# Optimization experiments

Hardware: AMD Instinct MI355X
Metric: run time of the kernel (lower is better)

## Reference

```python
import jax, jax.numpy as jnp
import numpy as np

H = 16  # num_heads


def setup_inputs() -> dict:
    key = jax.random.key(0)
    ks = jax.random.split(key, 8)
    B, S, d, L = 1, 2048, 1024, 8
    hd = d // H
    s = 0.02
    return {
        "x": jax.random.normal(ks[0], (B, S, d), jnp.float32),
        "past_values": jax.random.normal(ks[1], (L, B, H, S, hd), jnp.float32),
        "Wqkv": jax.random.normal(ks[2], (3 * d, d), jnp.float32) * s,
        "bqkv": jax.random.normal(ks[3], (3 * d,), jnp.float32) * s,
        "Wcol": jax.random.normal(ks[4], (d, d), jnp.float32) * s,
        "bcol": jax.random.normal(ks[5], (d,), jnp.float32) * s,
        "Wout": jax.random.normal(ks[6], (d, d), jnp.float32) * s,
        "bout": jax.random.normal(ks[7], (d,), jnp.float32) * s,
    }


def reference(x, past_values, Wqkv, bqkv, Wcol, bcol, Wout, bout):
    B, S, d = x.shape
    L = past_values.shape[0]
    hd = d // H
    scale = 1.0 / np.sqrt(hd).astype(np.float32)

    qkv = x @ Wqkv.T + bqkv                       # [B,S,3d]
    q, k, v = jnp.split(qkv, 3, axis=-1)

    def heads(t):                                  # [B,S,d] -> [B,H,S,hd]
        return t.reshape(B, S, H, hd).transpose(0, 2, 1, 3)

    q_row, k, v = heads(q), heads(k), heads(v)
    q_col = heads(x @ Wcol.T + bcol)

    # causal token scores [B,H,S,S]
    token_scores = jnp.einsum('bhqd,bhkd->bhqk', q_row, k) * scale
    causal = jnp.triu(jnp.ones((S, S), bool), 1)
    token_scores = jnp.where(causal, -jnp.inf, token_scores)

    # stack past values: torch stack(dim=3) -> [B,H,S,L,hd]; permute -> [B,S,L,H*hd]
    pv = past_values.transpose(1, 3, 0, 2, 4).reshape(B, S, L, d)
    ri = pv.reshape(B, S * L, d)
    mu = ri.mean(-1, keepdims=True)
    var = ri.var(-1, keepdims=True)
    ri = (ri - mu) / jnp.sqrt(var + 1e-5)          # F.layer_norm, no affine

    Wk, bk = Wqkv[d:2 * d], bqkv[d:2 * d]
    Wv, bv = Wqkv[2 * d:], bqkv[2 * d:]
    rk = (ri @ Wk.T + bk).reshape(B, S * L, H, hd).transpose(0, 2, 1, 3).reshape(B, H, S, L, hd)
    rv = (ri @ Wv.T + bv).reshape(B, S * L, H, hd).transpose(0, 2, 1, 3).reshape(B, H, S, L, hd)

    mem_scores = jnp.einsum('bhsd,bhsld->bhsl', q_col, rk) * scale  # [B,H,S,L]

    scores = jnp.concatenate([token_scores, mem_scores], axis=-1)   # [B,H,S,S+L]
    w = jax.nn.softmax(scores, axis=-1)
    tw, mw = w[..., :S], w[..., S:]

    ctx = jnp.einsum('bhqk,bhkd->bhqd', tw, v) + jnp.einsum('bhsl,bhsld->bhsd', mw, rv)
    out = ctx.transpose(0, 2, 1, 3).reshape(B, S, d)
    return out @ Wout.T + bout
```

## Files before the change

kernel.cpp:

```cpp
#include <hip/hip_runtime.h>
#include <math.h>

#define D   1024
#define H   16
#define HD  64
#define SEQ 2048
#define LL  8
#define SCALE 0.125f
#define TZS 1048

typedef __attribute__((ext_vector_type(8))) __bf16 bf16x8;
typedef __attribute__((ext_vector_type(4))) float floatx4;
typedef __attribute__((ext_vector_type(8))) unsigned short ushort8;

__device__ inline unsigned short f32_to_bf16(float f) {
    unsigned int u = __builtin_bit_cast(unsigned int, f);
    u += 0x7FFF + ((u >> 16) & 1);
    return (unsigned short)(u >> 16);
}
__device__ inline float bf2f(unsigned short u) {
    unsigned int x = (unsigned int)u << 16;
    return __builtin_bit_cast(float, x);
}
__device__ inline void load_lds16(const void* g, void* l) {
    __builtin_amdgcn_global_load_lds(
        (__attribute__((address_space(1))) void*)g,
        (__attribute__((address_space(3))) void*)l, 16, 0, 0);
}
__device__ inline void xcd_swizzle(int& bx, int& by) {
    const int gx   = gridDim.x;
    const int lin  = blockIdx.y * gx + blockIdx.x;
    const int nblk = gx * gridDim.y;
    const int virt = (lin & 7) * (nblk >> 3) + (lin >> 3);
    bx = virt % gx;
    by = virt / gx;
}

#define NQ_X    524288
#define NQ_WQKV 786432
#define NQ_WC   262144
#define LN_BLK  16384
#define CVT_BLK 7168
#define TR_BLK  256
#define PREP_GRID (LN_BLK + CVT_BLK + 4 + TR_BLK)

__global__ __launch_bounds__(256) void prep_kernel(
    const float* __restrict__ pv, const float* __restrict__ x,
    const float* __restrict__ Wqkv, const float* __restrict__ Wcol,
    const float* __restrict__ Wout, const float* __restrict__ bqkv,
    const float* __restrict__ bcol,
    unsigned short* __restrict__ ri, unsigned short* __restrict__ xb,
    unsigned short* __restrict__ W4b, unsigned short* __restrict__ Woutb,
    float* __restrict__ b4, unsigned short* __restrict__ WkT)
{
    __shared__ float ft[64][65];
    const int b = blockIdx.x;
    const int t = threadIdx.x;
    if (b < LN_BLK) {
        const int r = b;
        const int s = r >> 3, l = r & 7;
        const int h = t >> 4, e = (t & 15) * 4;
        const size_t src = (size_t)l * (H * SEQ * HD) + (size_t)h * (SEQ * HD)
                         + (size_t)s * HD + e;
        float4 v = *(const float4*)(pv + src);
        float sum = v.x + v.y + v.z + v.w;
        float sq  = v.x * v.x + v.y * v.y + v.z * v.z + v.w * v.w;
#pragma unroll
        for (int off = 32; off; off >>= 1) {
            sum += __shfl_xor(sum, off);
            sq  += __shfl_xor(sq, off);
        }
        __shared__ float red[8];
        if ((t & 63) == 0) { red[(t >> 6) * 2] = sum; red[(t >> 6) * 2 + 1] = sq; }
        __syncthreads();
        sum = red[0] + red[2] + red[4] + red[6];
        sq  = red[1] + red[3] + red[5] + red[7];
        const float mean = sum * (1.f / 1024.f);
        const float var  = sq * (1.f / 1024.f) - mean * mean;
        const float rstd = rsqrtf(var + 1e-5f);
        ushort4 o;
        o.x = f32_to_bf16((v.x - mean) * rstd);
        o.y = f32_to_bf16((v.y - mean) * rstd);
        o.z = f32_to_bf16((v.z - mean) * rstd);
        o.w = f32_to_bf16((v.w - mean) * rstd);
        *(ushort4*)(ri + (size_t)r * D + t * 4) = o;
    } else if (b < LN_BLK + CVT_BLK) {
        const int i = (b - LN_BLK) * 256 + t;
        const float* src; unsigned short* dst; int off;
        if (i < NQ_X) {
            src = x; dst = xb; off = i;
        } else if (i < NQ_X + NQ_WQKV) {
            src = Wqkv; dst = W4b; off = i - NQ_X;
        } else if (i < NQ_X + NQ_WQKV + NQ_WC) {
            src = Wcol; dst = W4b + (size_t)NQ_WQKV * 4; off = i - NQ_X - NQ_WQKV;
        } else {
            src = Wout; dst = Woutb; off = i - NQ_X - NQ_WQKV - NQ_WC;
        }
        float4 v = ((const float4*)src)[off];
        ushort4 o;
        o.x = f32_to_bf16(v.x); o.y = f32_to_bf16(v.y);
        o.z = f32_to_bf16(v.z); o.w = f32_to_bf16(v.w);
        ((ushort4*)dst)[off] = o;
    } else if (b < LN_BLK + CVT_BLK + 4) {
        const int q = (b - LN_BLK - CVT_BLK) * 256 + t;
        float4 v = (q < 768) ? ((const float4*)bqkv)[q] : ((const float4*)bcol)[q - 768];
        ((float4*)b4)[q] = v;
    } else {
        const int tt = b - LN_BLK - CVT_BLK - 4;
        const int kt = tt >> 4, et = tt & 15;
        const int r = t >> 2, c16 = (t & 3) * 16;
        const float* srow = Wqkv + (size_t)(1024 + et * 64 + r) * 1024 + kt * 64 + c16;
#pragma unroll
        for (int j = 0; j < 4; j++) {
            float4 v = *(const float4*)(srow + j * 4);
            ft[r][c16 + j * 4 + 0] = v.x; ft[r][c16 + j * 4 + 1] = v.y;
            ft[r][c16 + j * 4 + 2] = v.z; ft[r][c16 + j * 4 + 3] = v.w;
        }
        __syncthreads();
        const int rk = t >> 2, ec = (t & 3) * 16;
        unsigned short* orow = WkT + (size_t)(kt * 64 + rk) * 1024 + et * 64 + ec;
#pragma unroll
        for (int half = 0; half < 2; half++) {
            ushort8 o;
#pragma unroll
            for (int j = 0; j < 8; j++)
                o[j] = f32_to_bf16(ft[ec + half * 8 + j][rk]);
            *(ushort8*)(orow + half * 8) = o;
        }
    }
}

template <typename CT>
__global__ __launch_bounds__(256) void gemm_bf16_kernel(
    const unsigned short* __restrict__ A, const unsigned short* __restrict__ W,
    const float* __restrict__ bias, CT* __restrict__ C, int K, int N)
{
    __shared__ unsigned short As[128 * 32];
    __shared__ unsigned short Ws[128 * 32];
    const int t    = threadIdx.x;
    const int wave = t >> 6, lane = t & 63;
    const int wm   = wave >> 1, wn = wave & 1;
    int bx, by;
    xcd_swizzle(bx, by);
    const int m0 = by * 128, n0 = bx * 128;

    floatx4 acc[4][4];
#pragma unroll
    for (int i = 0; i < 4; i++)
#pragma unroll
        for (int j = 0; j < 4; j++) acc[i][j] = (floatx4)0.f;

    const int lrow = lane >> 2;
    const int lcol = (lane & 3) * 8;
    const unsigned short* Ag = A + (size_t)(m0 + wave * 32 + lrow) * K + lcol;
    const unsigned short* Wg = W + (size_t)(n0 + wave * 32 + lrow) * K + lcol;
    unsigned short* Asw = &As[wave * 32 * 32];
    unsigned short* Wsw = &Ws[wave * 32 * 32];
    const size_t rowskip = (size_t)16 * K;

    const int arow  = lane & 15;
    const int aquad = (lane >> 4) * 8;

    for (int k0 = 0; k0 < K; k0 += 32) {
        load_lds16(Ag + k0,           Asw);
        load_lds16(Ag + k0 + rowskip, Asw + 16 * 32);
        load_lds16(Wg + k0,           Wsw);
        load_lds16(Wg + k0 + rowskip, Wsw + 16 * 32);
        __syncthreads();

        bf16x8 af[4], wf[4];
#pragma unroll
        for (int mi = 0; mi < 4; mi++)
            af[mi] = *(const bf16x8*)&As[(wm * 64 + mi * 16 + arow) * 32 + aquad];
#pragma unroll
        for (int ni = 0; ni < 4; ni++)
            wf[ni] = *(const bf16x8*)&Ws[(wn * 64 + ni * 16 + arow) * 32 + aquad];
#pragma unroll
        for (int mi = 0; mi < 4; mi++)
#pragma unroll
            for (int ni = 0; ni < 4; ni++)
                acc[mi][ni] = __builtin_amdgcn_mfma_f32_16x16x32_bf16(
                    af[mi], wf[ni], acc[mi][ni], 0, 0, 0);
        __syncthreads();
    }

    const int crow = (lane >> 4) * 4, ccol = lane & 15;
#pragma unroll
    for (int mi = 0; mi < 4; mi++) {
#pragma unroll
        for (int ni = 0; ni < 4; ni++) {
            const int gm = m0 + wm * 64 + mi * 16 + crow;
            const int gn = n0 + wn * 64 + ni * 16 + ccol;
            const float bb = bias[gn];
#pragma unroll
            for (int r = 0; r < 4; r++) {
                float v = acc[mi][ni][r] + bb;
                if constexpr (sizeof(CT) == 2)
                    C[(size_t)(gm + r) * N + gn] = (CT)f32_to_bf16(v);
                else
                    C[(size_t)(gm + r) * N + gn] = v;
            }
        }
    }
}

__global__ __launch_bounds__(256, 2) void mem_attn_kernel(
    const unsigned short* __restrict__ qkv4, const unsigned short* __restrict__ ri,
    const unsigned short* __restrict__ WkT, const unsigned short* __restrict__ Wv,
    const float* __restrict__ bk, const float* __restrict__ bv,
    float* __restrict__ Omem, float2* __restrict__ mlmem)
{
    const int t = threadIdx.x;
    const int w = t >> 6, lane = t & 63;
    const int lrow = lane & 15, quad = lane >> 4, lk = quad * 8;
    const int b  = blockIdx.x;
    const int sg = (b & 7) + 8 * ((b >> 3) & 15);
    const int hg = b >> 7;
    const int s0 = sg * 16;
    const int r0 = s0 * 8;

    __shared__ unsigned short tz[2][16][TZS];
    __shared__ float s_sc[2][16][8];
    __shared__ float s_c[2][16];
    __shared__ float s_p[2][16][8];
    __shared__ float s_l2[2][16];

    {
        const int hh = t >> 7, s = (t >> 3) & 15, g = t & 7;
        const int h = hg * 2 + hh;
        const unsigned short* qc = qkv4 + (size_t)(s0 + s) * 4096 + 3072 + h * 64 + g * 8;
        ushort8 qv = *(const ushort8*)qc;
        float acc = 0.f;
#pragma unroll
        for (int j = 0; j < 8; j++)
            acc += bf2f(qv[j]) * bk[h * 64 + g * 8 + j];
        acc += __shfl_xor(acc, 1);
        acc += __shfl_xor(acc, 2);
        acc += __shfl_xor(acc, 4);
        if (g == 0) s_c[hh][s] = acc;
    }

    bf16x8 aq[2][2];
#pragma unroll
    for (int hh = 0; hh < 2; hh++)
#pragma unroll
        for (int kst = 0; kst < 2; kst++)
            aq[hh][kst] = *(const bf16x8*)(qkv4 + (size_t)(s0 + lrow) * 4096 + 3072
                                           + (hg * 2 + hh) * 64 + kst * 32 + lk);
#pragma unroll
    for (int hh = 0; hh < 2; hh++) {
        const int h = hg * 2 + hh;
#pragma unroll
        for (int nt = 0; nt < 16; nt++) {
            const int n = w * 256 + nt * 16;
            floatx4 acc = (floatx4)0.f;
#pragma unroll
            for (int kst = 0; kst < 2; kst++) {
                bf16x8 bw = *(const bf16x8*)(WkT + (size_t)(n + lrow) * 1024
                                             + h * 64 + kst * 32 + lk);
                acc = __builtin_amdgcn_mfma_f32_16x16x32_bf16(aq[hh][kst], bw, acc, 0, 0, 0);
            }
#pragma unroll
            for (int r = 0; r < 4; r++)
                tz[hh][quad * 4 + r][n + lrow] = f32_to_bf16(acc[r]);
        }
    }
    __syncthreads();

    {
        floatx4 sacc[2][2];
#pragma unroll
        for (int ntl = 0; ntl < 2; ntl++)
#pragma unroll
            for (int hh = 0; hh < 2; hh++) sacc[ntl][hh] = (floatx4)0.f;
        for (int kst = 0; kst < 32; kst++) {
            bf16x8 at0 = *(const bf16x8*)&tz[0][lrow][kst * 32 + lk];
            bf16x8 at1 = *(const bf16x8*)&tz[1][lrow][kst * 32 + lk];
#pragma unroll
            for (int ntl = 0; ntl < 2; ntl++) {
                bf16x8 br = *(const bf16x8*)(ri + (size_t)(r0 + w * 32 + ntl * 16 + lrow) * 1024
                                             + kst * 32 + lk);
                sacc[ntl][0] = __builtin_amdgcn_mfma_f32_16x16x32_bf16(at0, br, sacc[ntl][0], 0, 0, 0);
                sacc[ntl][1] = __builtin_amdgcn_mfma_f32_16x16x32_bf16(at1, br, sacc[ntl][1], 0, 0, 0);
            }
        }
        if (quad == w) {
            const int l = lrow & 7, hi = (lrow >> 3) & 1;
#pragma unroll
            for (int ntl = 0; ntl < 2; ntl++) {
                const int s = 4 * w + 2 * ntl + hi;
#pragma unroll
                for (int hh = 0; hh < 2; hh++) {
                    float val = hi ? sacc[ntl][hh][2 * ntl + 1] : sacc[ntl][hh][2 * ntl];
                    s_sc[hh][s][l] = val;
                }
            }
        }
    }
    __syncthreads();

    if (t < 32) {
        const int hh = t >> 4, s = t & 15;
        const int h = hg * 2 + hh;
        const float c = s_c[hh][s];
        float sc[8], m2 = -1e30f;
#pragma unroll
        for (int l = 0; l < 8; l++) {
            sc[l] = (s_sc[hh][s][l] + c) * SCALE;
            m2 = fmaxf(m2, sc[l]);
        }
        float l2 = 0.f;
#pragma unroll
        for (int l = 0; l < 8; l++) {
            float p = __expf(sc[l] - m2);
            s_p[hh][s][l] = p;
            l2 += p;
        }
        s_l2[hh][s] = l2;
        mlmem[(size_t)h * 2048 + s0 + s] = make_float2(m2, l2);
    }
    __syncthreads();

    {
        const int s = t & 15, kc = (t >> 4) * 64;
        float z0[64], z1[64];
#pragma unroll
        for (int j = 0; j < 64; j++) { z0[j] = 0.f; z1[j] = 0.f; }
        for (int l = 0; l < 8; l++) {
            const float p0 = s_p[0][s][l], p1 = s_p[1][s][l];
            const unsigned short* base = ri + (size_t)(r0 + s * 8 + l) * 1024 + kc;
#pragma unroll
            for (int c8 = 0; c8 < 8; c8++) {
                ushort8 v = *(const ushort8*)(base + c8 * 8);
#pragma unroll
                for (int j = 0; j < 8; j++) {
                    float f = bf2f(v[j]);
                    z0[c8 * 8 + j] = fmaf(p0, f, z0[c8 * 8 + j]);
                    z1[c8 * 8 + j] = fmaf(p1, f, z1[c8 * 8 + j]);
                }
            }
        }
        __syncthreads();
#pragma unroll
        for (int c8 = 0; c8 < 8; c8++) {
            ushort8 o0, o1;
#pragma unroll
            for (int j = 0; j < 8; j++) {
                o0[j] = f32_to_bf16(z0[c8 * 8 + j]);
                o1[j] = f32_to_bf16(z1[c8 * 8 + j]);
            }
            *(ushort8*)&tz[0][s][kc + c8 * 8] = o0;
            *(ushort8*)&tz[1][s][kc + c8 * 8] = o1;
        }
    }
    __syncthreads();

    {
        floatx4 oacc[2] = {(floatx4)0.f, (floatx4)0.f};
        for (int kst = 0; kst < 32; kst++) {
            bf16x8 az0 = *(const bf16x8*)&tz[0][lrow][kst * 32 + lk];
            bf16x8 az1 = *(const bf16x8*)&tz[1][lrow][kst * 32 + lk];
            bf16x8 bw0 = *(const bf16x8*)(Wv + (size_t)((hg * 2 + 0) * 64 + w * 16 + lrow) * 1024
                                          + kst * 32 + lk);
            bf16x8 bw1 = *(const bf16x8*)(Wv + (size_t)((hg * 2 + 1) * 64 + w * 16 + lrow) * 1024
                                          + kst * 32 + lk);
            oacc[0] = __builtin_amdgcn_mfma_f32_16x16x32_bf16(az0, bw0, oacc[0], 0, 0, 0);
            oacc[1] = __builtin_amdgcn_mfma_f32_16x16x32_bf16(az1, bw1, oacc[1], 0, 0, 0);
        }
        const int e = w * 16 + lrow;
#pragma unroll
        for (int hh = 0; hh < 2; hh++) {
            const int h = hg * 2 + hh;
            const float bve = bv[h * 64 + e];
#pragma unroll
            for (int r = 0; r < 4; r++) {
                const int s = quad * 4 + r;
                Omem[((size_t)h * 2048 + s0 + s) * 64 + e] =
                    oacc[hh][r] + s_l2[hh][s] * bve;
            }
        }
    }
}

__global__ __launch_bounds__(256) void attn_split_kernel(
    const unsigned short* __restrict__ qkv4,
    float* __restrict__ Opart, float2* __restrict__ mlpart)
{
    const int t    = threadIdx.x;
    const int w    = t >> 6, lane = t & 63;
    const int lrow = lane & 15;
    const int lk   = (lane >> 4) * 8;
    const int rrow = (lane >> 4) * 4;
    const int lin  = blockIdx.x;
    const int hs   = lin & 31, g = lin >> 5;
    const int h    = hs >> 1, s = hs & 1;
    const int a    = g & 7, bq = g >> 3;
    const int qt   = (bq == 0) ? a : (bq == 1) ? 15 - a : (bq == 2) ? 16 + a : 31 - a;
    const int q0   = qt * 64;
    const int n    = qt + 1, nh = (n + 1) >> 1;
    const int lo   = s ? nh : 0, hi = s ? n : nh;
    const int part = (h * 32 + qt) * 2 + s;

    __shared__ unsigned short Qs[64 * 72];
    __shared__ unsigned short Ks[64 * 72];
    __shared__ unsigned short Vt[64 * 72];
    __shared__ unsigned short Pb[64 * 72];

#pragma unroll
    for (int p = 0; p < 2; p++) {
        int idx = p * 256 + t;
        int row = idx >> 3, col = (idx & 7) * 8;
        *(bf16x8*)&Qs[row * 72 + col] =
            *(const bf16x8*)(qkv4 + (size_t)(q0 + row) * 4096 + h * HD + col);
    }

    float m_i[4], l_i[4];
    floatx4 Oacc[4];
#pragma unroll
    for (int r = 0; r < 4; r++) { m_i[r] = -1e30f; l_i[r] = 0.f; }
#pragma unroll
    for (int et = 0; et < 4; et++) Oacc[et] = (floatx4)0.f;

    for (int jt = lo; jt < hi; jt++) {
        const int j0 = jt * 64;
#pragma unroll
        for (int p = 0; p < 2; p++) {
            int idx = p * 256 + t;
            int row = idx >> 3, col = (idx & 7) * 8;
            *(bf16x8*)&Ks[row * 72 + col] =
                *(const bf16x8*)(qkv4 + (size_t)(j0 + row) * 4096 + D + h * HD + col);
        }
        {
            const int pr = t & 31, eg = t >> 5;
            const unsigned short* v0 =
                qkv4 + (size_t)(j0 + 2 * pr) * 4096 + 2 * D + h * HD + eg * 8;
            ushort8 va = *(const ushort8*)v0;
            ushort8 vb = *(const ushort8*)(v0 + 4096);
#pragma unroll
            for (int j = 0; j < 8; j++) {
                unsigned int pk = (unsigned int)va[j] | ((unsigned int)vb[j] << 16);
                *(unsigned int*)&Vt[(eg * 8 + j) * 72 + 2 * pr] = pk;
            }
        }
        __syncthreads();

        floatx4 S[4];
#pragma unroll
        for (int nt = 0; nt < 4; nt++) S[nt] = (floatx4)0.f;
#pragma unroll
        for (int kst = 0; kst < 2; kst++) {
            bf16x8 aqf = *(const bf16x8*)&Qs[(w * 16 + lrow) * 72 + kst * 32 + lk];
#pragma unroll
            for (int nt = 0; nt < 4; nt++) {
                bf16x8 bk = *(const bf16x8*)&Ks[(nt * 16 + lrow) * 72 + kst * 32 + lk];
                S[nt] = __builtin_amdgcn_mfma_f32_16x16x32_bf16(aqf, bk, S[nt], 0, 0, 0);
            }
        }

#pragma unroll
        for (int r = 0; r < 4; r++) {
            const int qg = q0 + w * 16 + rrow + r;
            float sc[4];
            float mx = -1e30f;
#pragma unroll
            for (int nt = 0; nt < 4; nt++) {
                sc[nt] = S[nt][r] * SCALE;
                if (j0 + nt * 16 + lrow > qg) sc[nt] = -1e30f;
                mx = fmaxf(mx, sc[nt]);
            }
#pragma unroll
            for (int off = 1; off < 16; off <<= 1)
                mx = fmaxf(mx, __shfl_xor(mx, off));
            if (mx <= -1e29f) {
#pragma unroll
                for (int nt = 0; nt < 4; nt++)
                    Pb[(w * 16 + rrow + r) * 72 + nt * 16 + lrow] = 0;
                continue;
            }
            const float newm  = fmaxf(m_i[r], mx);
            const float alpha = __expf(m_i[r] - newm);
            m_i[r] = newm;
            float ps = 0.f;
#pragma unroll
            for (int nt = 0; nt < 4; nt++) {
                float pe = __expf(sc[nt] - newm);
                ps += pe;
                Pb[(w * 16 + rrow + r) * 72 + nt * 16 + lrow] = f32_to_bf16(pe);
            }
#pragma unroll
            for (int off = 1; off < 16; off <<= 1)
                ps += __shfl_xor(ps, off);
            l_i[r] = l_i[r] * alpha + ps;
#pragma unroll
            for (int et = 0; et < 4; et++) Oacc[et][r] *= alpha;
        }
        __syncthreads();

#pragma unroll
        for (int kst = 0; kst < 2; kst++) {
            bf16x8 ap = *(const bf16x8*)&Pb[(w * 16 + lrow) * 72 + kst * 32 + lk];
#pragma unroll
            for (int et = 0; et < 4; et++) {
                bf16x8 bv = *(const bf16x8*)&Vt[(et * 16 + lrow) * 72 + kst * 32 + lk];
                Oacc[et] = __builtin_amdgcn_mfma_f32_16x16x32_bf16(ap, bv, Oacc[et], 0, 0, 0);
            }
        }
        __syncthreads();
    }

#pragma unroll
    for (int r = 0; r < 4; r++) {
        const int ql = w * 16 + rrow + r;
        if (lrow == 0) mlpart[(size_t)part * 64 + ql] = make_float2(m_i[r], l_i[r]);
#pragma unroll
        for (int et = 0; et < 4; et++)
            Opart[((size_t)part * 64 + ql) * 64 + et * 16 + lrow] = Oacc[et][r];
    }
}

__global__ __launch_bounds__(256) void attn_merge_kernel(
    const float* __restrict__ Opart, const float2* __restrict__ mlpart,
    const float* __restrict__ Omem, const float2* __restrict__ mlmem,
    unsigned short* __restrict__ ctx)
{
    const int blk = blockIdx.x;
    const int h = blk >> 5, qt = blk & 31;
    const int q0 = qt * 64;
    const int t = threadIdx.x, tx = t & 15, ty = t >> 4;
    const size_t p0 = (size_t)blk * 2, p1 = p0 + 1;
#pragma unroll
    for (int i = 0; i < 4; i++) {
        const int qi = ty * 4 + i, qg = q0 + qi;
        float2 ml0 = mlpart[p0 * 64 + qi];
        float2 ml1 = mlpart[p1 * 64 + qi];
        float2 mlm = mlmem[(size_t)h * 2048 + qg];
        const float M  = fmaxf(fmaxf(ml0.x, ml1.x), mlm.x);
        const float f0 = __expf(ml0.x - M), f1 = __expf(ml1.x - M), fm = __expf(mlm.x - M);
        const float rl = 1.f / (ml0.y * f0 + ml1.y * f1 + mlm.y * fm);
        float4 o0 = *(const float4*)&Opart[(p0 * 64 + qi) * 64 + tx * 4];
        float4 o1 = *(const float4*)&Opart[(p1 * 64 + qi) * 64 + tx * 4];
        float4 om = *(const float4*)&Omem[((size_t)h * 2048 + qg) * 64 + tx * 4];
        ushort4 ob;
        ob.x = f32_to_bf16((o0.x * f0 + o1.x * f1 + om.x * fm) * rl);
        ob.y = f32_to_bf16((o0.y * f0 + o1.y * f1 + om.y * fm) * rl);
        ob.z = f32_to_bf16((o0.z * f0 + o1.z * f1 + om.z * fm) * rl);
        ob.w = f32_to_bf16((o0.w * f0 + o1.w * f1 + om.w * fm) * rl);
        *(ushort4*)(ctx + (size_t)qg * D + h * HD + tx * 4) = ob;
    }
}

extern "C" void kernel_launch(void* const* d_in, const int* in_sizes, int n_in,
                              void* d_out, int out_size, void* d_ws, size_t ws_size,
                              hipStream_t stream)
{
    const float* x    = (const float*)d_in[0];
    const float* pv   = (const float*)d_in[1];
    const float* Wqkv = (const float*)d_in[2];
    const float* bqkv = (const float*)d_in[3];
    const float* Wcol = (const float*)d_in[4];
    const float* bcol = (const float*)d_in[5];
    const float* Wout = (const float*)d_in[6];
    const float* bout = (const float*)d_in[7];
    float* out = (float*)d_out;

    char* p = (char*)d_ws;
    unsigned short* x_bf    = (unsigned short*)p; p += (size_t)2048 * 1024 * 2;
    unsigned short* W4_bf   = (unsigned short*)p; p += (size_t)4096 * 1024 * 2;
    unsigned short* Wout_bf = (unsigned short*)p; p += (size_t)1024 * 1024 * 2;
    float*          b4      = (float*)p;          p += (size_t)4096 * 4;
    unsigned short* WkT_bf  = (unsigned short*)p; p += (size_t)1024 * 1024 * 2;
    unsigned short* ri_bf   = (unsigned short*)p; p += (size_t)16384 * 1024 * 2;
    unsigned short* qkv4_bf = (unsigned short*)p; p += (size_t)2048 * 4096 * 2;
    unsigned short* ctx_bf  = (unsigned short*)p; p += (size_t)2048 * 1024 * 2;
    float*          Opart   = (float*)p;          p += (size_t)1024 * 64 * 64 * 4;
    float2*         mlpart  = (float2*)p;         p += (size_t)1024 * 64 * 8;
    float*          Omem    = (float*)p;          p += (size_t)16 * 2048 * 64 * 4;
    float2*         mlmem   = (float2*)p;         p += (size_t)16 * 2048 * 8;

    prep_kernel<<<PREP_GRID, 256, 0, stream>>>(pv, x, Wqkv, Wcol, Wout, bqkv, bcol,
                                               ri_bf, x_bf, W4_bf, Wout_bf, b4, WkT_bf);
    gemm_bf16_kernel<unsigned short><<<dim3(32, 16), 256, 0, stream>>>(
        x_bf, W4_bf, b4, qkv4_bf, 1024, 4096);
    attn_split_kernel<<<1024, 256, 0, stream>>>(qkv4_bf, Opart, mlpart);
    mem_attn_kernel<<<1024, 256, 0, stream>>>(
        qkv4_bf, ri_bf, WkT_bf, W4_bf + (size_t)2048 * 1024,
        bqkv + 1024, bqkv + 2048, Omem, mlmem);
    attn_merge_kernel<<<512, 256, 0, stream>>>(Opart, mlpart, Omem, mlmem, ctx_bf);
    gemm_bf16_kernel<float><<<dim3(8, 16), 256, 0, stream>>>(
        ctx_bf, Wout_bf, bout, out, 1024, 1024);
}
```

Baseline: 370.0 us.

## Batch global loads in memory-attention GEMMs and prefetch K/V tiles in split attention

The memory-attention kernel's MFMA loops now issue several global loads of Wk, ri and Wv fragments at once before the MFMAs, so more loads are in flight. The weighted-sum phase now iterates column chunks with eight row loads each, which cuts the accumulator registers from 128 floats to 16. The split attention kernel prefetches the next K/V tile into registers while computing the current one, and drops two barriers per iteration by relying on per-wave ownership of Pb rows. The cost is higher register pressure from the prefetch buffers, plus correctness that now depends on those wave-private LDS access patterns.

After: 402.2 us. 1.09x slower.

```diff
diff --git a/kernel.cpp b/kernel.cpp
--- a/kernel.cpp
+++ b/kernel.cpp
@@ -251,18 +251,25 @@
     for (int hh = 0; hh < 2; hh++) {
         const int h = hg * 2 + hh;
 #pragma unroll
-        for (int nt = 0; nt < 16; nt++) {
-            const int n = w * 256 + nt * 16;
-            floatx4 acc = (floatx4)0.f;
-#pragma unroll
-            for (int kst = 0; kst < 2; kst++) {
-                bf16x8 bw = *(const bf16x8*)(WkT + (size_t)(n + lrow) * 1024
-                                             + h * 64 + kst * 32 + lk);
-                acc = __builtin_amdgcn_mfma_f32_16x16x32_bf16(aq[hh][kst], bw, acc, 0, 0, 0);
-            }
-#pragma unroll
-            for (int r = 0; r < 4; r++)
-                tz[hh][quad * 4 + r][n + lrow] = f32_to_bf16(acc[r]);
+        for (int ntq = 0; ntq < 4; ntq++) {
+            bf16x8 bw[4][2];
+#pragma unroll
+            for (int u = 0; u < 4; u++)
+#pragma unroll
+                for (int kst = 0; kst < 2; kst++)
+                    bw[u][kst] = *(const bf16x8*)(WkT
+                        + (size_t)(w * 256 + (ntq * 4 + u) * 16 + lrow) * 1024
+                        + h * 64 + kst * 32 + lk);
+#pragma unroll
+            for (int u = 0; u < 4; u++) {
+                floatx4 acc = (floatx4)0.f;
+                acc = __builtin_amdgcn_mfma_f32_16x16x32_bf16(aq[hh][0], bw[u][0], acc, 0, 0, 0);
+                acc = __builtin_amdgcn_mfma_f32_16x16x32_bf16(aq[hh][1], bw[u][1], acc, 0, 0, 0);
+                const int n = w * 256 + (ntq * 4 + u) * 16;
+#pragma unroll
+                for (int r = 0; r < 4; r++)
+                    tz[hh][quad * 4 + r][n + lrow] = f32_to_bf16(acc[r]);
+            }
         }
     }
     __syncthreads();
@@ -273,15 +280,25 @@
         for (int ntl = 0; ntl < 2; ntl++)
 #pragma unroll
             for (int hh = 0; hh < 2; hh++) sacc[ntl][hh] = (floatx4)0.f;
-        for (int kst = 0; kst < 32; kst++) {
-            bf16x8 at0 = *(const bf16x8*)&tz[0][lrow][kst * 32 + lk];
-            bf16x8 at1 = *(const bf16x8*)&tz[1][lrow][kst * 32 + lk];
-#pragma unroll
-            for (int ntl = 0; ntl < 2; ntl++) {
-                bf16x8 br = *(const bf16x8*)(ri + (size_t)(r0 + w * 32 + ntl * 16 + lrow) * 1024
-                                             + kst * 32 + lk);
-                sacc[ntl][0] = __builtin_amdgcn_mfma_f32_16x16x32_bf16(at0, br, sacc[ntl][0], 0, 0, 0);
-                sacc[ntl][1] = __builtin_amdgcn_mfma_f32_16x16x32_bf16(at1, br, sacc[ntl][1], 0, 0, 0);
+        const unsigned short* rb0 = ri + (size_t)(r0 + w * 32 + lrow) * 1024 + lk;
+        const unsigned short* rb1 = ri + (size_t)(r0 + w * 32 + 16 + lrow) * 1024 + lk;
+#pragma unroll
+        for (int kq = 0; kq < 8; kq++) {
+            bf16x8 r0v[4], r1v[4];
+#pragma unroll
+            for (int u = 0; u < 4; u++) {
+                r0v[u] = *(const bf16x8*)(rb0 + (kq * 4 + u) * 32);
+                r1v[u] = *(const bf16x8*)(rb1 + (kq * 4 + u) * 32);
+            }
+#pragma unroll
+            for (int u = 0; u < 4; u++) {
+                const int kst = kq * 4 + u;
+                bf16x8 at0 = *(const bf16x8*)&tz[0][lrow][kst * 32 + lk];
+                bf16x8 at1 = *(const bf16x8*)&tz[1][lrow][kst * 32 + lk];
+                sacc[0][0] = __builtin_amdgcn_mfma_f32_16x16x32_bf16(at0, r0v[u], sacc[0][0], 0, 0, 0);
+                sacc[0][1] = __builtin_amdgcn_mfma_f32_16x16x32_bf16(at1, r0v[u], sacc[0][1], 0, 0, 0);
+                sacc[1][0] = __builtin_amdgcn_mfma_f32_16x16x32_bf16(at0, r1v[u], sacc[1][0], 0, 0, 0);
+                sacc[1][1] = __builtin_amdgcn_mfma_f32_16x16x32_bf16(at1, r1v[u], sacc[1][1], 0, 0, 0);
             }
         }
         if (quad == w) {
@@ -323,31 +340,30 @@
 
     {
         const int s = t & 15, kc = (t >> 4) * 64;
-        float z0[64], z1[64];
-#pragma unroll
-        for (int j = 0; j < 64; j++) { z0[j] = 0.f; z1[j] = 0.f; }
-        for (int l = 0; l < 8; l++) {
-            const float p0 = s_p[0][s][l], p1 = s_p[1][s][l];
-            const unsigned short* base = ri + (size_t)(r0 + s * 8 + l) * 1024 + kc;
-#pragma unroll
-            for (int c8 = 0; c8 < 8; c8++) {
-                ushort8 v = *(const ushort8*)(base + c8 * 8);
+        const unsigned short* base = ri + (size_t)(r0 + s * 8) * 1024 + kc;
+        float p0[8], p1[8];
+#pragma unroll
+        for (int l = 0; l < 8; l++) { p0[l] = s_p[0][s][l]; p1[l] = s_p[1][s][l]; }
+#pragma unroll
+        for (int c8 = 0; c8 < 8; c8++) {
+            ushort8 v[8];
+#pragma unroll
+            for (int l = 0; l < 8; l++)
+                v[l] = *(const ushort8*)(base + (size_t)l * 1024 + c8 * 8);
+            float z0[8] = {0,0,0,0,0,0,0,0}, z1[8] = {0,0,0,0,0,0,0,0};
+#pragma unroll
+            for (int l = 0; l < 8; l++)
 #pragma unroll
                 for (int j = 0; j < 8; j++) {
-                    float f = bf2f(v[j]);
-                    z0[c8 * 8 + j] = fmaf(p0, f, z0[c8 * 8 + j]);
-                    z1[c8 * 8 + j] = fmaf(p1, f, z1[c8 * 8 + j]);
+                    float f = bf2f(v[l][j]);
+                    z0[j] = fmaf(p0[l], f, z0[j]);
+                    z1[j] = fmaf(p1[l], f, z1[j]);
                 }
-            }
-        }
-        __syncthreads();
-#pragma unroll
-        for (int c8 = 0; c8 < 8; c8++) {
             ushort8 o0, o1;
 #pragma unroll
             for (int j = 0; j < 8; j++) {
-                o0[j] = f32_to_bf16(z0[c8 * 8 + j]);
-                o1[j] = f32_to_bf16(z1[c8 * 8 + j]);
+                o0[j] = f32_to_bf16(z0[j]);
+                o1[j] = f32_to_bf16(z1[j]);
             }
             *(ushort8*)&tz[0][s][kc + c8 * 8] = o0;
             *(ushort8*)&tz[1][s][kc + c8 * 8] = o1;
@@ -357,15 +373,24 @@
 
     {
         floatx4 oacc[2] = {(floatx4)0.f, (floatx4)0.f};
-        for (int kst = 0; kst < 32; kst++) {
-            bf16x8 az0 = *(const bf16x8*)&tz[0][lrow][kst * 32 + lk];
-            bf16x8 az1 = *(const bf16x8*)&tz[1][lrow][kst * 32 + lk];
-            bf16x8 bw0 = *(const bf16x8*)(Wv + (size_t)((hg * 2 + 0) * 64 + w * 16 + lrow) * 1024
-                                          + kst * 32 + lk);
-            bf16x8 bw1 = *(const bf16x8*)(Wv + (size_t)((hg * 2 + 1) * 64 + w * 16 + lrow) * 1024
-                                          + kst * 32 + lk);
-            oacc[0] = __builtin_amdgcn_mfma_f32_16x16x32_bf16(az0, bw0, oacc[0], 0, 0, 0);
-            oacc[1] = __builtin_amdgcn_mfma_f32_16x16x32_bf16(az1, bw1, oacc[1], 0, 0, 0);
+        const unsigned short* wv0 = Wv + (size_t)((hg * 2 + 0) * 64 + w * 16 + lrow) * 1024 + lk;
+        const unsigned short* wv1 = Wv + (size_t)((hg * 2 + 1) * 64 + w * 16 + lrow) * 1024 + lk;
+#pragma unroll
+        for (int kq = 0; kq < 8; kq++) {
+            bf16x8 w0[4], w1[4];
+#pragma unroll
+            for (int u = 0; u < 4; u++) {
+                w0[u] = *(const bf16x8*)(wv0 + (kq * 4 + u) * 32);
+                w1[u] = *(const bf16x8*)(wv1 + (kq * 4 + u) * 32);
+            }
+#pragma unroll
+            for (int u = 0; u < 4; u++) {
+                const int kst = kq * 4 + u;
+                bf16x8 az0 = *(const bf16x8*)&tz[0][lrow][kst * 32 + lk];
+                bf16x8 az1 = *(const bf16x8*)&tz[1][lrow][kst * 32 + lk];
+                oacc[0] = __builtin_amdgcn_mfma_f32_16x16x32_bf16(az0, w0[u], oacc[0], 0, 0, 0);
+                oacc[1] = __builtin_amdgcn_mfma_f32_16x16x32_bf16(az1, w1[u], oacc[1], 0, 0, 0);
+            }
         }
         const int e = w * 16 + lrow;
 #pragma unroll
@@ -421,29 +446,32 @@
 #pragma unroll
     for (int et = 0; et < 4; et++) Oacc[et] = (floatx4)0.f;
 
+    const int krow = t >> 3, kcol = (t & 7) * 8;
+    const int vpr = t & 31, veg = t >> 5;
+    bf16x8 kr0, kr1;
+    ushort8 vr0, vr1;
+    auto preload = [&](int j0) {
+        kr0 = *(const bf16x8*)(qkv4 + (size_t)(j0 + krow) * 4096 + D + h * HD + kcol);
+        kr1 = *(const bf16x8*)(qkv4 + (size_t)(j0 + krow + 32) * 4096 + D + h * HD + kcol);
+        const unsigned short* v0 = qkv4 + (size_t)(j0 + 2 * vpr) * 4096 + 2 * D + h * HD + veg * 8;
+        vr0 = *(const ushort8*)v0;
+        vr1 = *(const ushort8*)(v0 + 4096);
+    };
+    if (lo < hi) preload(lo * 64);
+
     for (int jt = lo; jt < hi; jt++) {
+        __syncthreads();
+        *(bf16x8*)&Ks[krow * 72 + kcol] = kr0;
+        *(bf16x8*)&Ks[(krow + 32) * 72 + kcol] = kr1;
+#pragma unroll
+        for (int j = 0; j < 8; j++) {
+            unsigned int pk = (unsigned int)vr0[j] | ((unsigned int)vr1[j] << 16);
+            *(unsigned int*)&Vt[(veg * 8 + j) * 72 + 2 * vpr] = pk;
+        }
+        if (jt + 1 < hi) preload((jt + 1) * 64);
+        __syncthreads();
+
         const int j0 = jt * 64;
-#pragma unroll
-        for (int p = 0; p < 2; p++) {
-            int idx = p * 256 + t;
-            int row = idx >> 3, col = (idx & 7) * 8;
-            *(bf16x8*)&Ks[row * 72 + col] =
-                *(const bf16x8*)(qkv4 + (size_t)(j0 + row) * 4096 + D + h * HD + col);
-        }
-        {
-            const int pr = t & 31, eg = t >> 5;
-            const unsigned short* v0 =
-                qkv4 + (size_t)(j0 + 2 * pr) * 4096 + 2 * D + h * HD + eg * 8;
-            ushort8 va = *(const ushort8*)v0;
-            ushort8 vb = *(const ushort8*)(v0 + 4096);
-#pragma unroll
-            for (int j = 0; j < 8; j++) {
-                unsigned int pk = (unsigned int)va[j] | ((unsigned int)vb[j] << 16);
-                *(unsigned int*)&Vt[(eg * 8 + j) * 72 + 2 * pr] = pk;
-            }
-        }
-        __syncthreads();
-
         floatx4 S[4];
 #pragma unroll
         for (int nt = 0; nt < 4; nt++) S[nt] = (floatx4)0.f;
@@ -494,7 +522,6 @@
 #pragma unroll
             for (int et = 0; et < 4; et++) Oacc[et][r] *= alpha;
         }
-        __syncthreads();
 
 #pragma unroll
         for (int kst = 0; kst < 2; kst++) {
@@ -505,7 +532,6 @@
                 Oacc[et] = __builtin_amdgcn_mfma_f32_16x16x32_bf16(ap, bv, Oacc[et], 0, 0, 0);
             }
         }
-        __syncthreads();
     }
 
 #pragma unroll
```
